# Performance work log

Measured on AMD Instinct MI355X. Metric: run time of the kernel, lower is better.

## Reference

```python
import jax, jax.numpy as jnp
import numpy as np

NUM_HEADS = 8

def _ln(x, w, b, eps=1e-5):
    m = x.mean(-1, keepdims=True)
    v = ((x - m) ** 2).mean(-1, keepdims=True)
    return (x - m) / jnp.sqrt(v + eps) * w + b

def _conv3(x, w, b):
    y = jax.lax.conv_general_dilated(x, w, (1, 1), 'SAME',
                                     dimension_numbers=('NCHW', 'OIHW', 'NCHW'))
    return y + b[None, :, None, None]

def _pos_encoding(c, h, w, dtype):
    # first c//2 channels: x position in [0,1]; next c//2: y position
    px = jnp.broadcast_to(jnp.linspace(0, 1, w, dtype=dtype)[None, :], (h, w))
    py = jnp.broadcast_to(jnp.linspace(0, 1, h, dtype=dtype)[:, None], (h, w))
    pe = jnp.concatenate([jnp.broadcast_to(px, (c // 2, h, w)),
                          jnp.broadcast_to(py, (c // 2, h, w))], axis=0)
    return pe[None]  # [1,c,h,w]

def _pixel_shuffle(x, r=2):
    b, c4, h, w = x.shape
    c = c4 // (r * r)
    return x.reshape(b, c, r, r, h, w).transpose(0, 1, 4, 2, 5, 3).reshape(b, c, h * r, w * r)

def _forward(x, text_hidden, proj_w, proj_b, cf_w, cf_b,
             blk_qw, blk_qb, blk_kw, blk_kb, blk_vw, blk_vb,
             blk_ow, blk_ob, blk_ln1w, blk_ln1b, blk_ln2w, blk_ln2b,
             up_w, up_b, cl_w, cl_b):
    B = x.shape[0]
    # text projection: [B, L, text_dim] -> [B, L, C]
    tf = jnp.einsum('bld,cd->blc', text_hidden, proj_w) + proj_b
    feat = _conv3(x, cf_w, cf_b)  # [B, C, H, W]
    _, C, H, W = feat.shape
    L = tf.shape[1]
    hd = C // NUM_HEADS
    scale = hd ** (-0.5)
    pe = _pos_encoding(C, H, W, feat.dtype)

    def block(feat, p):
        qw, qb, kw, kb, vw, vb, ow, ob, l1w, l1b, l2w, l2b = p
        q = jnp.einsum('oi,bihw->bohw', qw, feat) + qb[None, :, None, None]
        q = q + pe * 0.05
        q_flat = q.reshape(B, C, H * W).transpose(0, 2, 1)  # [B, HW, C]
        q_norm = _ln(q_flat, l1w, l1b)
        qh = q_norm.reshape(B, H * W, NUM_HEADS, hd).transpose(0, 2, 1, 3)
        k = jnp.einsum('blc,oc->blo', tf, kw) + kb
        v = jnp.einsum('blc,oc->blo', tf, vw) + vb
        kn = _ln(k, l2w, l2b)
        kh = kn.reshape(B, L, NUM_HEADS, hd).transpose(0, 2, 1, 3)
        vh = v.reshape(B, L, NUM_HEADS, hd).transpose(0, 2, 1, 3)
        attn = jax.nn.softmax(jnp.einsum('bhnd,bhld->bhnl', qh, kh) * scale, axis=-1)
        out = jnp.einsum('bhnl,bhld->bhnd', attn, vh)          # [B, H8, HW, hd]
        out = out.transpose(0, 2, 1, 3).reshape(B, H * W, C)   # [B, HW, C]
        out = out.transpose(0, 2, 1).reshape(B, C, H, W)
        out = jnp.einsum('oi,bihw->bohw', ow, out) + ob[None, :, None, None]
        return out + feat, None

    blk_params = (blk_qw, blk_qb, blk_kw, blk_kb, blk_vw, blk_vb,
                  blk_ow, blk_ob, blk_ln1w, blk_ln1b, blk_ln2w, blk_ln2b)
    feat, _ = jax.lax.scan(block, feat, blk_params)

    for i in range(up_w.shape[0]):
        feat = jax.nn.relu(_pixel_shuffle(_conv3(feat, up_w[i], up_b[i]), 2))
    return _conv3(feat, cl_w, cl_b)


def setup_inputs() -> dict:
    key = jax.random.key(0)
    ks = jax.random.split(key, 20)
    B, H, W = 8, 64, 64
    C, D, L, NB = 64, 512, 77, 16
    s = 0.05
    inp = {
        'x': jax.random.normal(ks[0], (B, 3, H, W), jnp.float32),
        'text_hidden': jax.random.normal(ks[1], (B, L, D), jnp.float32),
        'proj_w': jax.random.normal(ks[2], (C, D), jnp.float32) * 0.01,
        'proj_b': jnp.zeros((C,), jnp.float32),
        'cf_w': jax.random.normal(ks[3], (C, 3, 3, 3), jnp.float32) * s,
        'cf_b': jnp.zeros((C,), jnp.float32),
        'blk_qw': jax.random.normal(ks[4], (NB, C, C), jnp.float32) * s,
        'blk_qb': jnp.zeros((NB, C), jnp.float32),
        'blk_kw': jax.random.normal(ks[5], (NB, C, C), jnp.float32) * 0.01,
        'blk_kb': jnp.zeros((NB, C), jnp.float32),
        'blk_vw': jax.random.normal(ks[6], (NB, C, C), jnp.float32) * 0.01,
        'blk_vb': jnp.zeros((NB, C), jnp.float32),
        'blk_ow': jax.random.normal(ks[7], (NB, C, C), jnp.float32) * s,
        'blk_ob': jnp.zeros((NB, C), jnp.float32),
        'blk_ln1w': jnp.ones((NB, C), jnp.float32),
        'blk_ln1b': jnp.zeros((NB, C), jnp.float32),
        'blk_ln2w': jnp.ones((NB, C), jnp.float32),
        'blk_ln2b': jnp.zeros((NB, C), jnp.float32),
        'up_w': jax.random.normal(ks[8], (2, C * 4, C, 3, 3), jnp.float32) * s,
        'up_b': jnp.zeros((2, C * 4), jnp.float32),
        'cl_w': jax.random.normal(ks[9], (3, C, 3, 3), jnp.float32) * s,
        'cl_b': jnp.zeros((3,), jnp.float32),
    }
    return inp


def reference(x, text_hidden, proj_w, proj_b, cf_w, cf_b,
              blk_qw, blk_qb, blk_kw, blk_kb, blk_vw, blk_vb,
              blk_ow, blk_ob, blk_ln1w, blk_ln1b, blk_ln2w, blk_ln2b,
              up_w, up_b, cl_w, cl_b):
    return _forward(x, text_hidden, proj_w, proj_b, cf_w, cf_b,
                    blk_qw, blk_qb, blk_kw, blk_kb, blk_vw, blk_vb,
                    blk_ow, blk_ob, blk_ln1w, blk_ln1b, blk_ln2w, blk_ln2b,
                    up_w, up_b, cl_w, cl_b)
```

## Files before the change

kernel.cpp:

```cpp
#include <hip/hip_runtime.h>
#include <math.h>

#define BATCH 8
#define C 64
#define NH 8
#define HD 8
#define LTXT 77
#define H0 64
#define W0 64
#define HW0 (H0*W0)

typedef __attribute__((ext_vector_type(8))) short bfrag;
typedef __attribute__((ext_vector_type(4))) float ffrag;
typedef __attribute__((ext_vector_type(8))) unsigned short us8;
typedef __attribute__((ext_vector_type(4))) unsigned short us4;
typedef __attribute__((ext_vector_type(2))) float f2;

#if defined(__has_builtin)
#if __has_builtin(__builtin_amdgcn_exp2f)
#define EXP2(x) __builtin_amdgcn_exp2f(x)
#else
#define EXP2(x) exp2f(x)
#endif
#if __has_builtin(__builtin_amdgcn_fdot2_f32_bf16)
#define USE_DOT2 1
typedef __bf16 bf2v __attribute__((ext_vector_type(2)));
#endif
#else
#define EXP2(x) exp2f(x)
#endif

__device__ __forceinline__ unsigned short f2bf(float f) {
    unsigned u = __builtin_bit_cast(unsigned, f);
    u += 0x7fff + ((u >> 16) & 1);
    return (unsigned short)(u >> 16);
}

__device__ __forceinline__ f2 bfp2f2(unsigned w) {
    f2 r;
    r[0] = __builtin_bit_cast(float, w << 16);
    r[1] = __builtin_bit_cast(float, w & 0xffff0000u);
    return r;
}

__global__ void text_proj_kernel(const float* __restrict__ th, const float* __restrict__ pw,
                                 const float* __restrict__ pb, float* __restrict__ tf) {
    __shared__ float sh[512];
    int bl = blockIdx.x;
    int c = threadIdx.x;
    const float* row = th + (size_t)bl * 512;
    for (int i = c; i < 512; i += 64) sh[i] = row[i];
    __syncthreads();
    const float* wrow = pw + c * 512;
    float acc = pb[c];
    for (int i = 0; i < 512; i += 4) {
        acc += sh[i] * wrow[i] + sh[i+1] * wrow[i+1] + sh[i+2] * wrow[i+2] + sh[i+3] * wrow[i+3];
    }
    tf[bl * 64 + c] = acc;
}

__global__ void __launch_bounds__(256)
prep_kernel(const float* __restrict__ x, const float* __restrict__ cf_w,
            const float* __restrict__ cf_b, float* __restrict__ feat,
            const float* __restrict__ up_w,
            unsigned short* __restrict__ PW1, unsigned short* __restrict__ PW2,
            const float* __restrict__ cl_w, unsigned short* __restrict__ PWF,
            const float* __restrict__ qw, const float* __restrict__ ow,
            unsigned short* __restrict__ PQ, unsigned short* __restrict__ PO) {
    int blk = blockIdx.x;
    if (blk < 8192) {
        int idx = blk * 256 + threadIdx.x;
        int wx = idx & 63;
        int h = (idx >> 6) & 63;
        int o = (idx >> 12) & 63;
        int b = idx >> 18;
        const float* wr = cf_w + o * 27;
        float acc = cf_b[o];
        for (int ci = 0; ci < 3; ci++) {
            for (int ky = 0; ky < 3; ky++) {
                int y = h + ky - 1;
                if ((unsigned)y >= 64u) continue;
                const float* xr = x + (((size_t)b * 3 + ci) * 64 + y) * 64;
                const float* wk = wr + ci * 9 + ky * 3;
                if (wx > 0) acc += xr[wx - 1] * wk[0];
                acc += xr[wx] * wk[1];
                if (wx < 63) acc += xr[wx + 1] * wk[2];
            }
        }
        feat[idx] = acc;
    } else if (blk < 8192 + 1152) {
        int e0 = blk - 8192;
        int st = e0 / 576;
        int e = (e0 % 576) * 256 + threadIdx.x;
        const float* w = up_w + (size_t)st * 147456;
        unsigned short* d = st ? PW2 : PW1;
        int j = e & 7, n = (e >> 3) & 255, q = (e >> 11) & 3, s = (e >> 13) & 1, t = e >> 14;
        int c = n & 63, g = n >> 6;
        int co = 4 * c + g, ci = 32 * s + 8 * q + j;
        d[e] = f2bf(w[co * 576 + ci * 9 + t]);
    } else if (blk < 8192 + 1152 + 36) {
        int e = (blk - 8192 - 1152) * 256 + threadIdx.x;
        int j = e & 7, n = (e >> 3) & 15, q = (e >> 7) & 3, s = (e >> 9) & 1, t = e >> 10;
        int ci = 32 * s + 8 * q + j;
        float v = (n < 3) ? cl_w[n * 576 + ci * 9 + t] : 0.f;
        PWF[e] = f2bf(v);
    } else {
        int e = (blk - 8192 - 1152 - 36) * 256 + threadIdx.x;
        int j = e & 7, n = (e >> 3) & 63, quad = (e >> 9) & 3, kt = (e >> 11) & 1, layer = e >> 12;
        int c = kt * 32 + quad * 8 + j;
        PQ[e] = f2bf(qw[layer * 4096 + n * 64 + c]);
        PO[e] = f2bf(ow[layer * 4096 + n * 64 + c]);
    }
}

__global__ void kv_all_kernel(const float* __restrict__ tf,
                              const float* __restrict__ kw, const float* __restrict__ kb,
                              const float* __restrict__ vw, const float* __restrict__ vb,
                              const float* __restrict__ l2w, const float* __restrict__ l2b,
                              unsigned short* __restrict__ kvi) {
    __shared__ float sh[64];
    int g = blockIdx.x;
    int bl = g % (BATCH * LTXT);
    int blk = g / (BATCH * LTXT);
    int o = threadIdx.x;
    sh[o] = tf[bl * 64 + o];
    __syncthreads();
    const float* kr = kw + blk * 4096 + o * 64;
    const float* vr = vw + blk * 4096 + o * 64;
    float ka = kb[blk * 64 + o], va = vb[blk * 64 + o];
    for (int c2 = 0; c2 < 64; c2++) {
        float t = sh[c2];
        ka += t * kr[c2];
        va += t * vr[c2];
    }
    float s = ka;
    for (int off = 32; off; off >>= 1) s += __shfl_xor(s, off, 64);
    float mean = s * (1.0f / 64.0f);
    float d = ka - mean;
    float s2 = d * d;
    for (int off = 32; off; off >>= 1) s2 += __shfl_xor(s2, off, 64);
    float rstd = rsqrtf(s2 * (1.0f / 64.0f) + 1e-5f);
    float kn = (d * rstd * l2w[blk * 64 + o] + l2b[blk * 64 + o]) * 0.51006973f;
    size_t base = ((size_t)blk * (BATCH * LTXT) + bl) * 128;
    int hd = o >> 3, ch = o & 7;
    kvi[base + hd * 16 + ch]     = f2bf(kn);
    kvi[base + hd * 16 + 8 + ch] = f2bf(va);
}

__global__ void __launch_bounds__(1024, 8)
attn_all_kernel(const float* __restrict__ feat,
                const unsigned short* __restrict__ kvi,
                const unsigned short* __restrict__ PQ, const unsigned short* __restrict__ PO,
                const float* __restrict__ qb_a, const float* __restrict__ ob_a,
                const float* __restrict__ l1w_a, const float* __restrict__ l1b_a,
                unsigned short* __restrict__ X1) {
    __shared__ __attribute__((aligned(16))) unsigned short sfb[64][72];
    __shared__ __attribute__((aligned(16))) unsigned short sob[64][72];
    __shared__ __attribute__((aligned(16))) float qf[64][68];
    __shared__ float so[64][64];
    __shared__ __attribute__((aligned(16))) float red[2][4][64];
    __shared__ float ss1[8][64];
    __shared__ __attribute__((aligned(16))) unsigned short skv[LTXT * 128];

    int b = blockIdx.x >> 6;
    int tile = blockIdx.x & 63;
    int n0 = tile << 6;
    int wv = __builtin_amdgcn_readfirstlane(threadIdx.x >> 6);
    int lane = threadIdx.x & 63;
    int p = lane;
    int quad = lane >> 4, n16 = lane & 15;
    int mt = wv >> 2, nt = wv & 3;
    int o0 = wv * 4;
    int h = wv >> 1, half = wv & 1;
    int a0 = h * 8;
    const float* fbase = feat + ((size_t)b << 18) + n0;

    float rres[4];
#pragma unroll
    for (int j = 0; j < 4; j++) rres[j] = fbase[(o0 + j) * HW0 + p];
    {
        us4 v;
#pragma unroll
        for (int j = 0; j < 4; j++) v[j] = f2bf(rres[j]);
        *(us4*)&sfb[p][o0] = v;
    }

    const float pxk = 0.05f / 63.0f;
    float py005 = (float)tile * pxk;
    __syncthreads();

#pragma unroll 1
    for (int layer = 0; layer < 16; layer++) {
        const float* qb = qb_a + layer * 64;
        const float* ob = ob_a + layer * 64;
        const float* l1w = l1w_a + layer * 64;
        const float* l1b = l1b_a + layer * 64;

        {
            const us8* gk = (const us8*)(kvi + (((size_t)layer * BATCH + b) * LTXT) * 128);
            us8* sk = (us8*)skv;
            int e = threadIdx.x;
            us8 c0 = gk[e];
            us8 c1 = (e + 1024 < 1232) ? gk[e + 1024] : c0;
            sk[e] = c0;
            if (e + 1024 < 1232) sk[e + 1024] = c1;
        }

        {
            bfrag af0 = *(const bfrag*)&sfb[mt * 16 + n16][quad * 8];
            bfrag af1 = *(const bfrag*)&sfb[mt * 16 + n16][32 + quad * 8];
            const unsigned short* bq = PQ + layer * 4096 + (size_t)((quad * 64) + nt * 16 + n16) * 8;
            bfrag bf0 = *(const bfrag*)bq;
            bfrag bf1 = *(const bfrag*)(bq + 2048);
            ffrag cc = (ffrag)0.f;
            cc = __builtin_amdgcn_mfma_f32_16x16x32_bf16(af0, bf0, cc, 0, 0, 0);
            cc = __builtin_amdgcn_mfma_f32_16x16x32_bf16(af1, bf1, cc, 0, 0, 0);
            int cch = nt * 16 + n16;
            float qbv = qb[cch];
            int p0 = mt * 16 + quad * 4;
            float pe0 = (nt < 2) ? (float)p0 * pxk : py005;
            float ped = (nt < 2) ? pxk : 0.f;
            float ov[4];
            ov[0] = cc[0] + qbv + pe0;
            ov[1] = cc[1] + qbv + pe0 + ped;
            ov[2] = cc[2] + qbv + pe0 + 2.f * ped;
            ov[3] = cc[3] + qbv + pe0 + 3.f * ped;
            float4 o4 = {ov[0], ov[1], ov[2], ov[3]};
            *(float4*)&qf[cch][p0] = o4;

            float sv[4], sq[4];
#pragma unroll
            for (int r = 0; r < 4; r++) {
                float s = ov[r], s2v = ov[r] * ov[r];
                s += __shfl_xor(s, 1);  s2v += __shfl_xor(s2v, 1);
                s += __shfl_xor(s, 2);  s2v += __shfl_xor(s2v, 2);
                s += __shfl_xor(s, 4);  s2v += __shfl_xor(s2v, 4);
                s += __shfl_xor(s, 8);  s2v += __shfl_xor(s2v, 8);
                sv[r] = s; sq[r] = s2v;
            }
            if (n16 == 0) {
                *(float4*)&red[0][nt][p0] = (float4){sv[0], sv[1], sv[2], sv[3]};
                *(float4*)&red[1][nt][p0] = (float4){sq[0], sq[1], sq[2], sq[3]};
            }
        }
        __syncthreads();

        {
            float ts = red[0][0][p] + red[0][1][p] + red[0][2][p] + red[0][3][p];
            float ts2 = red[1][0][p] + red[1][1][p] + red[1][2][p] + red[1][3][p];
            float mean = ts * (1.0f / 64.0f);
            float var = ts2 * (1.0f / 64.0f) - mean * mean;
            float rstd = rsqrtf(var + 1e-5f);

#if defined(USE_DOT2)
            unsigned qp[4];
#pragma unroll
            for (int j = 0; j < 4; j++) {
                float qa  = (qf[a0 + 2 * j][p]     - mean) * rstd * l1w[a0 + 2 * j]     + l1b[a0 + 2 * j];
                float qbv = (qf[a0 + 2 * j + 1][p] - mean) * rstd * l1w[a0 + 2 * j + 1] + l1b[a0 + 2 * j + 1];
                qp[j] = (unsigned)f2bf(qa) | ((unsigned)f2bf(qbv) << 16);
            }
#define QKDOT(kk) ({ \
    float dd = 0.f; \
    dd = __builtin_amdgcn_fdot2_f32_bf16(__builtin_bit_cast(bf2v, (kk).x), __builtin_bit_cast(bf2v, qp[0]), dd, false); \
    dd = __builtin_amdgcn_fdot2_f32_bf16(__builtin_bit_cast(bf2v, (kk).y), __builtin_bit_cast(bf2v, qp[1]), dd, false); \
    dd = __builtin_amdgcn_fdot2_f32_bf16(__builtin_bit_cast(bf2v, (kk).z), __builtin_bit_cast(bf2v, qp[2]), dd, false); \
    dd = __builtin_amdgcn_fdot2_f32_bf16(__builtin_bit_cast(bf2v, (kk).w), __builtin_bit_cast(bf2v, qp[3]), dd, false); \
    dd; })
#else
            f2 qv[4];
#pragma unroll
            for (int j = 0; j < 4; j++) {
                float qa  = (qf[a0 + 2 * j][p]     - mean) * rstd * l1w[a0 + 2 * j]     + l1b[a0 + 2 * j];
                float qbv = (qf[a0 + 2 * j + 1][p] - mean) * rstd * l1w[a0 + 2 * j + 1] + l1b[a0 + 2 * j + 1];
                qv[j][0] = qa;
                qv[j][1] = qbv;
            }
#define QKDOT(kk) ({ \
    f2 d2 = qv[0] * bfp2f2((kk).x); \
    d2 += qv[1] * bfp2f2((kk).y); \
    d2 += qv[2] * bfp2f2((kk).z); \
    d2 += qv[3] * bfp2f2((kk).w); \
    d2[0] + d2[1]; })
#endif
            const unsigned short* kvl = &skv[h * 16];
            int l0 = half ? 39 : 0;
            int l1 = half ? 77 : 39;
            float ssum = 0.f;
            f2 acc2[4] = {(f2)0.f, (f2)0.f, (f2)0.f, (f2)0.f};
            int l = l0;
            for (; l + 2 <= l1; l += 2) {
                uint4 ka = *(const uint4*)(kvl + (size_t)l * 128);
                uint4 va = *(const uint4*)(kvl + (size_t)l * 128 + 8);
                uint4 kb2 = *(const uint4*)(kvl + (size_t)(l + 1) * 128);
                uint4 vb2 = *(const uint4*)(kvl + (size_t)(l + 1) * 128 + 8);

                float ea = EXP2(QKDOT(ka));
                ssum += ea;
                f2 ea2 = {ea, ea};
                acc2[0] += ea2 * bfp2f2(va.x);
                acc2[1] += ea2 * bfp2f2(va.y);
                acc2[2] += ea2 * bfp2f2(va.z);
                acc2[3] += ea2 * bfp2f2(va.w);

                float eb = EXP2(QKDOT(kb2));
                ssum += eb;
                f2 eb2 = {eb, eb};
                acc2[0] += eb2 * bfp2f2(vb2.x);
                acc2[1] += eb2 * bfp2f2(vb2.y);
                acc2[2] += eb2 * bfp2f2(vb2.z);
                acc2[3] += eb2 * bfp2f2(vb2.w);
            }
            if (l < l1) {
                uint4 kc = *(const uint4*)(kvl + (size_t)l * 128);
                uint4 vc = *(const uint4*)(kvl + (size_t)l * 128 + 8);
                float e = EXP2(QKDOT(kc));
                ssum += e;
                f2 e2 = {e, e};
                acc2[0] += e2 * bfp2f2(vc.x);
                acc2[1] += e2 * bfp2f2(vc.y);
                acc2[2] += e2 * bfp2f2(vc.z);
                acc2[3] += e2 * bfp2f2(vc.w);
            }
#undef QKDOT
            if (half) {
#pragma unroll
                for (int j = 0; j < 4; j++) {
                    so[a0 + 2 * j][p] = acc2[j][0];
                    so[a0 + 2 * j + 1][p] = acc2[j][1];
                }
                ss1[h][p] = ssum;
            }
            __syncthreads();
            if (!half) {
                float inv = 1.0f / (ssum + ss1[h][p]);
                us8 v;
#pragma unroll
                for (int j = 0; j < 4; j++) {
                    v[2*j]   = f2bf((acc2[j][0] + so[a0 + 2*j][p]) * inv);
                    v[2*j+1] = f2bf((acc2[j][1] + so[a0 + 2*j+1][p]) * inv);
                }
                *(us8*)&sob[p][a0] = v;
            }
        }
        __syncthreads();

        {
            bfrag af0 = *(const bfrag*)&sob[mt * 16 + n16][quad * 8];
            bfrag af1 = *(const bfrag*)&sob[mt * 16 + n16][32 + quad * 8];
            const unsigned short* bo = PO + layer * 4096 + (size_t)((quad * 64) + nt * 16 + n16) * 8;
            bfrag bf0 = *(const bfrag*)bo;
            bfrag bf1 = *(const bfrag*)(bo + 2048);
            ffrag cc = (ffrag)0.f;
            cc = __builtin_amdgcn_mfma_f32_16x16x32_bf16(af0, bf0, cc, 0, 0, 0);
            cc = __builtin_amdgcn_mfma_f32_16x16x32_bf16(af1, bf1, cc, 0, 0, 0);
            int cch = nt * 16 + n16;
            float obv = ob[cch];
            int p0 = mt * 16 + quad * 4;
            float4 o4;
            o4.x = cc[0] + obv; o4.y = cc[1] + obv; o4.z = cc[2] + obv; o4.w = cc[3] + obv;
            *(float4*)&qf[cch][p0] = o4;
        }
        __syncthreads();

        {
            us4 v;
#pragma unroll
            for (int j = 0; j < 4; j++) {
                rres[j] += qf[o0 + j][p];
                v[j] = f2bf(rres[j]);
            }
            *(us4*)&sfb[p][o0] = v;
        }
        __syncthreads();
    }

    us4 v;
#pragma unroll
    for (int j = 0; j < 4; j++) v[j] = f2bf(rres[j]);
    *(us4*)(X1 + ((size_t)(b * 4096 + n0 + p)) * 64 + o0) = v;
}

__global__ void __launch_bounds__(512)
upconv_mfma_kernel(const unsigned short* __restrict__ X, const unsigned short* __restrict__ Bp,
                   const float* __restrict__ bias, unsigned short* __restrict__ Y,
                   int Hin, int Win) {
    __shared__ __attribute__((aligned(16))) unsigned short sx[3 * 66 * 72];

    int wv = threadIdx.x >> 6;
    int lane = threadIdx.x & 63;
    int q = lane >> 4, n16 = lane & 15;
    int m0 = blockIdx.x * 64;
    int hw = Hin * Win;
    int b = m0 / hw, rem = m0 % hw;
    int h = rem / Win, w0 = rem % Win;
    const unsigned short* Xb = X + (size_t)b * hw * 64;

    const us8 z8 = (us8)(unsigned short)0;
    for (int e = threadIdx.x; e < 1584; e += 512) {
        int ch8 = e & 7;
        int pxi = (e >> 3) % 66;
        int row = e / 528;
        int hh = h + row - 1, wp = w0 + pxi - 1;
        us8 v = z8;
        if ((unsigned)hh < (unsigned)Hin && (unsigned)wp < (unsigned)Win)
            v = *(const us8*)(Xb + ((size_t)hh * Win + wp) * 64 + ch8 * 8);
        *(us8*)&sx[row * 4752 + pxi * 72 + ch8 * 8] = v;
    }
    __syncthreads();

    ffrag acc[4][2];
#pragma unroll
    for (int i = 0; i < 4; i++)
#pragma unroll
        for (int j2 = 0; j2 < 2; j2++) acc[i][j2] = (ffrag)0.f;

    int npb = wv * 32;

    for (int t = 0; t < 9; t++) {
        int dy = t / 3, dx = t % 3;
        bfrag af[4][2];
#pragma unroll
        for (int mt = 0; mt < 4; mt++) {
            const unsigned short* sp = &sx[dy * 4752 + (mt * 16 + n16 + dx) * 72 + q * 8];
            af[mt][0] = *(const bfrag*)sp;
            af[mt][1] = *(const bfrag*)(sp + 32);
        }
#pragma unroll
        for (int s = 0; s < 2; s++) {
#pragma unroll
            for (int nt = 0; nt < 2; nt++) {
                bfrag bf = *(const bfrag*)(Bp + (size_t)((((t * 2 + s) * 4 + q) * 256) + npb + nt * 16 + n16) * 8);
#pragma unroll
                for (int mt = 0; mt < 4; mt++)
                    acc[mt][nt] = __builtin_amdgcn_mfma_f32_16x16x32_bf16(af[mt][s], bf, acc[mt][nt], 0, 0, 0);
            }
        }
    }

    int g = wv >> 1;
    int r1 = wv >> 2, r2 = (wv >> 1) & 1;
    int cbase = (wv & 1) * 32;
    float bv[2];
#pragma unroll
    for (int nt = 0; nt < 2; nt++) bv[nt] = bias[4 * (cbase + nt * 16 + n16) + g];
    int Wo = Win * 2;
    unsigned short* Yb = Y + ((size_t)b * Hin * 2 * Wo + (size_t)(2 * h + r1) * Wo + r2) * 64;
#pragma unroll
    for (int mt = 0; mt < 4; mt++) {
#pragma unroll
        for (int r = 0; r < 4; r++) {
            int m = mt * 16 + q * 4 + r;
            unsigned short* dst = Yb + (size_t)(2 * (w0 + m)) * 64;
#pragma unroll
            for (int nt = 0; nt < 2; nt++) {
                float v = acc[mt][nt][r] + bv[nt];
                v = fmaxf(v, 0.f);
                dst[cbase + nt * 16 + n16] = f2bf(v);
            }
        }
    }
}

__global__ void __launch_bounds__(256)
final_mfma_kernel(const unsigned short* __restrict__ X, const unsigned short* __restrict__ Bp,
                  const float* __restrict__ bias, float* __restrict__ out) {
    __shared__ __attribute__((aligned(16))) unsigned short sx[6 * 66 * 72];

    int t0 = blockIdx.x;
    int wseg = t0 & 3;
    int rg = (t0 >> 2) & 63;
    int b = t0 >> 8;
    int y0 = rg * 4, w0 = wseg * 64;
    int wv = threadIdx.x >> 6, lane = threadIdx.x & 63;
    int q = lane >> 4, n16 = lane & 15;
    const unsigned short* Xb = X + (size_t)b * 65536 * 64;

    const us8 z8 = (us8)(unsigned short)0;
    for (int e = threadIdx.x; e < 3168; e += 256) {
        int ch8 = e & 7;
        int pxi = (e >> 3) % 66;
        int row = e / 528;
        int hh = y0 - 1 + row, wp = w0 - 1 + pxi;
        us8 v = z8;
        if ((unsigned)hh < 256u && (unsigned)wp < 256u)
            v = *(const us8*)(Xb + ((size_t)hh * 256 + wp) * 64 + ch8 * 8);
        *(us8*)&sx[row * 4752 + pxi * 72 + ch8 * 8] = v;
    }
    __syncthreads();

    ffrag acc[4];
#pragma unroll
    for (int i = 0; i < 4; i++) acc[i] = (ffrag)0.f;

    for (int t = 0; t < 9; t++) {
        int dy = t / 3, dx = t % 3;
        bfrag af[4][2];
#pragma unroll
        for (int mt = 0; mt < 4; mt++) {
            const unsigned short* sp = &sx[(wv + dy) * 4752 + (mt * 16 + n16 + dx) * 72 + q * 8];
            af[mt][0] = *(const bfrag*)sp;
            af[mt][1] = *(const bfrag*)(sp + 32);
        }
#pragma unroll
        for (int s = 0; s < 2; s++) {
            bfrag bf = *(const bfrag*)(Bp + (size_t)((((t * 2 + s) * 4 + q) * 16) + n16) * 8);
#pragma unroll
            for (int mt = 0; mt < 4; mt++)
                acc[mt] = __builtin_amdgcn_mfma_f32_16x16x32_bf16(af[mt][s], bf, acc[mt], 0, 0, 0);
        }
    }

    if (n16 < 3) {
        float bj = bias[n16];
        float* ob = out + (((size_t)b * 3 + n16) * 256 + (y0 + wv)) * 256;
#pragma unroll
        for (int mt = 0; mt < 4; mt++)
#pragma unroll
            for (int r = 0; r < 4; r++)
                ob[w0 + mt * 16 + q * 4 + r] = acc[mt][r] + bj;
    }
}

extern "C" void kernel_launch(void* const* d_in, const int* in_sizes, int n_in,
                              void* d_out, int out_size, void* d_ws, size_t ws_size,
                              hipStream_t stream) {
    const float* x      = (const float*)d_in[0];
    const float* th     = (const float*)d_in[1];
    const float* proj_w = (const float*)d_in[2];
    const float* proj_b = (const float*)d_in[3];
    const float* cf_w   = (const float*)d_in[4];
    const float* cf_b   = (const float*)d_in[5];
    const float* qw     = (const float*)d_in[6];
    const float* qb     = (const float*)d_in[7];
    const float* kw     = (const float*)d_in[8];
    const float* kb     = (const float*)d_in[9];
    const float* vw     = (const float*)d_in[10];
    const float* vb     = (const float*)d_in[11];
    const float* ow     = (const float*)d_in[12];
    const float* ob     = (const float*)d_in[13];
    const float* l1w    = (const float*)d_in[14];
    const float* l1b    = (const float*)d_in[15];
    const float* l2w    = (const float*)d_in[16];
    const float* l2b    = (const float*)d_in[17];
    const float* up_w   = (const float*)d_in[18];
    const float* up_b   = (const float*)d_in[19];
    const float* cl_w   = (const float*)d_in[20];
    const float* cl_b   = (const float*)d_in[21];

    float* ws   = (float*)d_ws;
    float* feat = ws;
    float* tf   = feat + 2097152;
    unsigned short* kvi = (unsigned short*)(tf + 39424);
    unsigned short* X1  = kvi + 1261568;
    unsigned short* X2  = X1 + 2097152;
    unsigned short* X3  = X2 + 8388608;
    unsigned short* PW1 = X3 + 33554432;
    unsigned short* PW2 = PW1 + 147456;
    unsigned short* PWF = PW2 + 147456;
    unsigned short* PQ  = PWF + 9216;
    unsigned short* PO  = PQ + 65536;

    hipLaunchKernelGGL(prep_kernel, dim3(8192 + 1152 + 36 + 256), dim3(256), 0, stream,
                       x, cf_w, cf_b, feat, up_w, PW1, PW2, cl_w, PWF, qw, ow, PQ, PO);
    hipLaunchKernelGGL(text_proj_kernel, dim3(BATCH * LTXT), dim3(64), 0, stream,
                       th, proj_w, proj_b, tf);
    hipLaunchKernelGGL(kv_all_kernel, dim3(16 * BATCH * LTXT), dim3(64), 0, stream,
                       tf, kw, kb, vw, vb, l2w, l2b, kvi);

    hipLaunchKernelGGL(attn_all_kernel, dim3(BATCH * (HW0 / 64)), dim3(1024), 0, stream,
                       feat, kvi, PQ, PO, qb, ob, l1w, l1b, X1);

    hipLaunchKernelGGL(upconv_mfma_kernel, dim3(BATCH * 64 * 64 / 64), dim3(512), 0, stream,
                       X1, PW1, up_b, X2, 64, 64);
    hipLaunchKernelGGL(upconv_mfma_kernel, dim3(BATCH * 128 * 128 / 64), dim3(512), 0, stream,
                       X2, PW2, up_b + 256, X3, 128, 128);
    hipLaunchKernelGGL(final_mfma_kernel, dim3(BATCH * 64 * 4), dim3(256), 0, stream,
                       X3, PWF, cl_b, (float*)d_out);
}
```

Baseline: 542.1 us.

## Read K/V directly from global memory in attention, store V in fp32

Drops the per-layer copy of interleaved bf16 K/V into shared memory, along with its LDS footprint. The attention loop now reads bf16 K and fp32 V straight from global (wave-uniform addresses, cache-resident) in separate planar buffers. The loop is unrolled by three. V stays in fp32, which removes the bf16 unpack and improves accuracy, but roughly doubles V bytes and relies on scalar or L1 cache hits in place of LDS.

```diff
diff --git a/kernel.cpp b/kernel.cpp
--- a/kernel.cpp
+++ b/kernel.cpp
@@ -117,7 +117,7 @@
                               const float* __restrict__ kw, const float* __restrict__ kb,
                               const float* __restrict__ vw, const float* __restrict__ vb,
                               const float* __restrict__ l2w, const float* __restrict__ l2b,
-                              unsigned short* __restrict__ kvi) {
+                              unsigned short* __restrict__ kb16, float* __restrict__ vbuf) {
     __shared__ float sh[64];
     int g = blockIdx.x;
     int bl = g % (BATCH * LTXT);
@@ -141,15 +141,14 @@
     for (int off = 32; off; off >>= 1) s2 += __shfl_xor(s2, off, 64);
     float rstd = rsqrtf(s2 * (1.0f / 64.0f) + 1e-5f);
     float kn = (d * rstd * l2w[blk * 64 + o] + l2b[blk * 64 + o]) * 0.51006973f;
-    size_t base = ((size_t)blk * (BATCH * LTXT) + bl) * 128;
-    int hd = o >> 3, ch = o & 7;
-    kvi[base + hd * 16 + ch]     = f2bf(kn);
-    kvi[base + hd * 16 + 8 + ch] = f2bf(va);
+    size_t ti = (size_t)blk * (BATCH * LTXT) + bl;
+    kb16[ti * 64 + o] = f2bf(kn);
+    vbuf[ti * 64 + o] = va;
 }
 
 __global__ void __launch_bounds__(1024, 8)
 attn_all_kernel(const float* __restrict__ feat,
-                const unsigned short* __restrict__ kvi,
+                const unsigned short* __restrict__ kb16, const float* __restrict__ vbuf,
                 const unsigned short* __restrict__ PQ, const unsigned short* __restrict__ PO,
                 const float* __restrict__ qb_a, const float* __restrict__ ob_a,
                 const float* __restrict__ l1w_a, const float* __restrict__ l1b_a,
@@ -160,7 +159,6 @@
     __shared__ float so[64][64];
     __shared__ __attribute__((aligned(16))) float red[2][4][64];
     __shared__ float ss1[8][64];
-    __shared__ __attribute__((aligned(16))) unsigned short skv[LTXT * 128];
 
     int b = blockIdx.x >> 6;
     int tile = blockIdx.x & 63;
@@ -195,16 +193,6 @@
         const float* ob = ob_a + layer * 64;
         const float* l1w = l1w_a + layer * 64;
         const float* l1b = l1b_a + layer * 64;
-
-        {
-            const us8* gk = (const us8*)(kvi + (((size_t)layer * BATCH + b) * LTXT) * 128);
-            us8* sk = (us8*)skv;
-            int e = threadIdx.x;
-            us8 c0 = gk[e];
-            us8 c1 = (e + 1024 < 1232) ? gk[e + 1024] : c0;
-            sk[e] = c0;
-            if (e + 1024 < 1232) sk[e + 1024] = c1;
-        }
 
         {
             bfrag af0 = *(const bfrag*)&sfb[mt * 16 + n16][quad * 8];
@@ -283,44 +271,60 @@
     d2 += qv[3] * bfp2f2((kk).w); \
     d2[0] + d2[1]; })
 #endif
-            const unsigned short* kvl = &skv[h * 16];
+            size_t tbase = (size_t)layer * BATCH * LTXT + (size_t)b * LTXT;
+            const unsigned short* kb_b = kb16 + tbase * 64 + a0;
+            const float* vb_b = vbuf + tbase * 64 + a0;
             int l0 = half ? 39 : 0;
             int l1 = half ? 77 : 39;
             float ssum = 0.f;
             f2 acc2[4] = {(f2)0.f, (f2)0.f, (f2)0.f, (f2)0.f};
             int l = l0;
-            for (; l + 2 <= l1; l += 2) {
-                uint4 ka = *(const uint4*)(kvl + (size_t)l * 128);
-                uint4 va = *(const uint4*)(kvl + (size_t)l * 128 + 8);
-                uint4 kb2 = *(const uint4*)(kvl + (size_t)(l + 1) * 128);
-                uint4 vb2 = *(const uint4*)(kvl + (size_t)(l + 1) * 128 + 8);
-
-                float ea = EXP2(QKDOT(ka));
+            for (; l + 3 <= l1; l += 3) {
+                uint4  kA = *(const uint4*)(kb_b + (size_t)l * 64);
+                uint4  kB = *(const uint4*)(kb_b + (size_t)(l + 1) * 64);
+                uint4  kC = *(const uint4*)(kb_b + (size_t)(l + 2) * 64);
+                float4 vA0 = *(const float4*)(vb_b + (size_t)l * 64);
+                float4 vA1 = *(const float4*)(vb_b + (size_t)l * 64 + 4);
+                float4 vB0 = *(const float4*)(vb_b + (size_t)(l + 1) * 64);
+                float4 vB1 = *(const float4*)(vb_b + (size_t)(l + 1) * 64 + 4);
+                float4 vC0 = *(const float4*)(vb_b + (size_t)(l + 2) * 64);
+                float4 vC1 = *(const float4*)(vb_b + (size_t)(l + 2) * 64 + 4);
+
+                float ea = EXP2(QKDOT(kA));
                 ssum += ea;
                 f2 ea2 = {ea, ea};
-                acc2[0] += ea2 * bfp2f2(va.x);
-                acc2[1] += ea2 * bfp2f2(va.y);
-                acc2[2] += ea2 * bfp2f2(va.z);
-                acc2[3] += ea2 * bfp2f2(va.w);
-
-                float eb = EXP2(QKDOT(kb2));
+                acc2[0] += ea2 * (f2){vA0.x, vA0.y};
+                acc2[1] += ea2 * (f2){vA0.z, vA0.w};
+                acc2[2] += ea2 * (f2){vA1.x, vA1.y};
+                acc2[3] += ea2 * (f2){vA1.z, vA1.w};
+
+                float eb = EXP2(QKDOT(kB));
                 ssum += eb;
                 f2 eb2 = {eb, eb};
-                acc2[0] += eb2 * bfp2f2(vb2.x);
-                acc2[1] += eb2 * bfp2f2(vb2.y);
-                acc2[2] += eb2 * bfp2f2(vb2.z);
-                acc2[3] += eb2 * bfp2f2(vb2.w);
-            }
-            if (l < l1) {
-                uint4 kc = *(const uint4*)(kvl + (size_t)l * 128);
-                uint4 vc = *(const uint4*)(kvl + (size_t)l * 128 + 8);
-                float e = EXP2(QKDOT(kc));
+                acc2[0] += eb2 * (f2){vB0.x, vB0.y};
+                acc2[1] += eb2 * (f2){vB0.z, vB0.w};
+                acc2[2] += eb2 * (f2){vB1.x, vB1.y};
+                acc2[3] += eb2 * (f2){vB1.z, vB1.w};
+
+                float ec = EXP2(QKDOT(kC));
+                ssum += ec;
+                f2 ec2 = {ec, ec};
+                acc2[0] += ec2 * (f2){vC0.x, vC0.y};
+                acc2[1] += ec2 * (f2){vC0.z, vC0.w};
+                acc2[2] += ec2 * (f2){vC1.x, vC1.y};
+                acc2[3] += ec2 * (f2){vC1.z, vC1.w};
+            }
+            for (; l < l1; l++) {
+                uint4  kD = *(const uint4*)(kb_b + (size_t)l * 64);
+                float4 vD0 = *(const float4*)(vb_b + (size_t)l * 64);
+                float4 vD1 = *(const float4*)(vb_b + (size_t)l * 64 + 4);
+                float e = EXP2(QKDOT(kD));
                 ssum += e;
                 f2 e2 = {e, e};
-                acc2[0] += e2 * bfp2f2(vc.x);
-                acc2[1] += e2 * bfp2f2(vc.y);
-                acc2[2] += e2 * bfp2f2(vc.z);
-                acc2[3] += e2 * bfp2f2(vc.w);
+                acc2[0] += e2 * (f2){vD0.x, vD0.y};
+                acc2[1] += e2 * (f2){vD0.z, vD0.w};
+                acc2[2] += e2 * (f2){vD1.x, vD1.y};
+                acc2[3] += e2 * (f2){vD1.z, vD1.w};
             }
 #undef QKDOT
             if (half) {
@@ -551,8 +555,9 @@
     float* ws   = (float*)d_ws;
     float* feat = ws;
     float* tf   = feat + 2097152;
-    unsigned short* kvi = (unsigned short*)(tf + 39424);
-    unsigned short* X1  = kvi + 1261568;
+    float* vbuf = tf + 39424;
+    unsigned short* kb16 = (unsigned short*)(vbuf + 630784);
+    unsigned short* X1  = kb16 + 630784;
     unsigned short* X2  = X1 + 2097152;
     unsigned short* X3  = X2 + 8388608;
     unsigned short* PW1 = X3 + 33554432;
@@ -566,10 +571,10 @@
     hipLaunchKernelGGL(text_proj_kernel, dim3(BATCH * LTXT), dim3(64), 0, stream,
                        th, proj_w, proj_b, tf);
     hipLaunchKernelGGL(kv_all_kernel, dim3(16 * BATCH * LTXT), dim3(64), 0, stream,
-                       tf, kw, kb, vw, vb, l2w, l2b, kvi);
+                       tf, kw, kb, vw, vb, l2w, l2b, kb16, vbuf);
 
     hipLaunchKernelGGL(attn_all_kernel, dim3(BATCH * (HW0 / 64)), dim3(1024), 0, stream,
-                       feat, kvi, PQ, PO, qb, ob, l1w, l1b, X1);
+                       feat, kb16, vbuf, PQ, PO, qb, ob, l1w, l1b, X1);
 
     hipLaunchKernelGGL(upconv_mfma_kernel, dim3(BATCH * 64 * 64 / 64), dim3(512), 0, stream,
                        X1, PW1, up_b, X2, 64, 64);
```

New measurement: 488.7 us. -9.8%, faster.
